# Optimization experiments

Hardware: AMD Instinct MI355X
Metric: run time of the kernel (lower is better)

Reference implementation:

```python
import jax, jax.numpy as jnp
import numpy as np

N_THRESH = 100  # thresholds = 0.00, 0.01, ..., 0.99


def setup_inputs() -> dict:
    key = jax.random.key(0)
    k1, k2 = jax.random.split(key)
    predicted_mask = jax.random.uniform(k1, (32, 1, 1024, 1024), dtype=jnp.float32)
    gt_mask = jax.random.randint(k2, (32, 1, 1024, 1024), 0, 2, dtype=jnp.int32)
    return {"predicted_mask": predicted_mask, "gt_mask": gt_mask}


def reference(predicted_mask, gt_mask):
    # Single-pass histogram formulation of: for each t_k in arange(0,1,0.01),
    # iou_k = |(pred > t_k) & gt| / |(pred > t_k) | gt|  (torchmetrics binary Jaccard,
    # strict '>' thresholding, safe-divide -> 0 when union is empty).
    thresholds = jnp.arange(0.0, 1.0, 0.01, dtype=jnp.float32)  # [100], sorted
    pred = jnp.squeeze(predicted_mask).ravel()                  # [N] probabilities in [0,1]
    gt = jnp.squeeze(gt_mask).ravel().astype(jnp.float32)       # [N] 0/1

    # cnt[i] = number of thresholds strictly below pred[i]; pixel i satisfies
    # (pred > t_k) exactly for k in [0, cnt[i]).
    cnt = jnp.searchsorted(thresholds, pred, side='left')       # [N] int in [0, 100]

    hist_pos = jax.ops.segment_sum(gt, cnt, num_segments=N_THRESH + 1)              # [101]
    hist_all = jax.ops.segment_sum(jnp.ones_like(gt), cnt, num_segments=N_THRESH + 1)

    # TP_k = #{pred > t_k and gt==1} = sum_{c > k} hist_pos[c]  (suffix sums via cumsum)
    tp = jnp.sum(hist_pos) - jnp.cumsum(hist_pos)[:N_THRESH]        # [100]
    pred_pos = jnp.sum(hist_all) - jnp.cumsum(hist_all)[:N_THRESH]  # [100] #{pred > t_k}
    n_gt_pos = jnp.sum(gt)

    union = pred_pos + n_gt_pos - tp                                 # TP + FP + FN
    ious = jnp.where(union > 0, tp / jnp.maximum(union, 1.0), 0.0)   # safe divide -> 0
    return thresholds, ious
```

## Files before the change

### kernel.cpp

```cpp
#include <hip/hip_runtime.h>

#define N_THRESH 100
#define NBINS 101
#define TPB 384
#define GRID 1024
#define FLUSH_GROUPS 29

__global__ void zero_ws_kernel(unsigned long long* __restrict__ ws) {
    int i = threadIdx.x;
    if (i < NBINS + 1) ws[i] = 0ull;
}

__device__ __forceinline__ int bin_of(float v) {
    int e = (int)(v * 100.0f);
    e = e < 0 ? 0 : (e > 99 ? 99 : e);
    double ed = (double)e * 0.01;
    float t0 = (float)ed;
    float t1 = (float)(ed + 0.01);
    int c = e + (t0 < v ? 1 : 0) + (t1 < v ? 1 : 0);
    return c > N_THRESH ? N_THRESH : c;
}

__device__ __forceinline__ void bump(unsigned short* h, int tid, float v, int g) {
    h[bin_of(v) * TPB + tid] += (unsigned short)(1u + (g != 0 ? 256u : 0u));
}

__device__ __forceinline__ void fold_row(const unsigned short* h, int r,
                                         unsigned long long& acc_c,
                                         unsigned long long& acc_p) {
    const unsigned int* row = (const unsigned int*)(h + r * TPB);
    unsigned int c = 0, p = 0;
    for (int j = 0; j < TPB / 2; ++j) {
        int jj = j + r; if (jj >= TPB / 2) jj -= TPB / 2;
        unsigned int v = row[jj];
        c += (v & 0xffu) + ((v >> 16) & 0xffu);
        p += ((v >> 8) & 0xffu) + ((v >> 24) & 0xffu);
    }
    acc_c += c; acc_p += p;
}

#define PROCESS16(PA, PB, PC, PD, GA, GB, GC, GD) do {            \
    bump(sA, tid, (PA).x, (GA).x); bump(sB, tid, (PA).y, (GA).y); \
    bump(sA, tid, (PA).z, (GA).z); bump(sB, tid, (PA).w, (GA).w); \
    bump(sA, tid, (PB).x, (GB).x); bump(sB, tid, (PB).y, (GB).y); \
    bump(sA, tid, (PB).z, (GB).z); bump(sB, tid, (PB).w, (GB).w); \
    bump(sA, tid, (PC).x, (GC).x); bump(sB, tid, (PC).y, (GC).y); \
    bump(sA, tid, (PC).z, (GC).z); bump(sB, tid, (PC).w, (GC).w); \
    bump(sA, tid, (PD).x, (GD).x); bump(sB, tid, (PD).y, (GD).y); \
    bump(sA, tid, (PD).z, (GD).z); bump(sB, tid, (PD).w, (GD).w); \
} while (0)

__global__ __launch_bounds__(TPB) void hist_kernel(
        const float* __restrict__ pred,
        const int* __restrict__ gt,
        unsigned long long* __restrict__ ws,
        float* __restrict__ out,
        int n) {
    __shared__ unsigned short sA[NBINS * TPB];
    __shared__ unsigned short sB[NBINS * TPB];
    __shared__ unsigned int fpos[NBINS], fall[NBINS];
    __shared__ int is_last;

    const int tid = threadIdx.x;
    unsigned int* const za = (unsigned int*)sA;
    unsigned int* const zb = (unsigned int*)sB;

    for (int i = tid; i < NBINS * (TPB / 2); i += TPB) { za[i] = 0u; zb[i] = 0u; }
    __syncthreads();

    const int nvec = n >> 2;
    const float4* __restrict__ p4 = (const float4*)pred;
    const int4*   __restrict__ g4 = (const int4*)gt;
    const int gsz = gridDim.x * blockDim.x;
    const int i0  = blockIdx.x * blockDim.x + tid;
    const int iters  = nvec / gsz;
    const int groups = iters >> 2;

    unsigned long long acc_c = 0ull, acc_p = 0ull;

    int gs = 0;
    while (gs < groups) {
        const int ge = (groups < gs + FLUSH_GROUPS) ? groups : gs + FLUSH_GROUPS;
        int j = i0 + gs * 4 * gsz;
        float4 pa = p4[j], pb = p4[j + gsz], pc = p4[j + 2 * gsz], pd = p4[j + 3 * gsz];
        int4   ga = g4[j], gb = g4[j + gsz], gc = g4[j + 2 * gsz], gd = g4[j + 3 * gsz];
        for (int g = gs + 1; g < ge; ++g) {
            j = i0 + g * 4 * gsz;
            float4 qa = p4[j], qb = p4[j + gsz], qc = p4[j + 2 * gsz], qd = p4[j + 3 * gsz];
            int4   ra = g4[j], rb = g4[j + gsz], rc = g4[j + 2 * gsz], rd = g4[j + 3 * gsz];
            PROCESS16(pa, pb, pc, pd, ga, gb, gc, gd);
            pa = qa; pb = qb; pc = qc; pd = qd;
            ga = ra; gb = rb; gc = rc; gd = rd;
        }
        PROCESS16(pa, pb, pc, pd, ga, gb, gc, gd);
        gs = ge;
        if (gs < groups) {
            __syncthreads();
            if (tid < NBINS)                            fold_row(sA, tid, acc_c, acc_p);
            else if (tid >= 192 && tid < 192 + NBINS)   fold_row(sB, tid - 192, acc_c, acc_p);
            __syncthreads();
            for (int i = tid; i < NBINS * (TPB / 2); i += TPB) { za[i] = 0u; zb[i] = 0u; }
            __syncthreads();
        }
    }

    for (int k = groups * 4; ; ++k) {
        int i = i0 + k * gsz;
        if (i >= nvec) break;
        float4 p = p4[i]; int4 g = g4[i];
        bump(sA, tid, p.x, g.x); bump(sB, tid, p.y, g.y);
        bump(sA, tid, p.z, g.z); bump(sB, tid, p.w, g.w);
    }

    if (blockIdx.x == 0 && tid == 0) {
        for (int k = nvec << 2; k < n; ++k) {
            int b = bin_of(pred[k]);
            sA[b * TPB] = (unsigned short)(sA[b * TPB] + 1u + (gt[k] != 0 ? 256u : 0u));
        }
    }

    __syncthreads();
    if (tid >= 192 && tid < 192 + NBINS) {
        fold_row(sB, tid - 192, acc_c, acc_p);
        fall[tid - 192] = (unsigned int)acc_c;
        fpos[tid - 192] = (unsigned int)acc_p;
    }
    __syncthreads();
    if (tid < NBINS) {
        fold_row(sA, tid, acc_c, acc_p);
        unsigned long long cnt = acc_c + fall[tid];
        unsigned long long pos = acc_p + fpos[tid];
        if (cnt | pos) atomicAdd(&ws[tid], (pos << 32) | cnt);
        __threadfence();
    }
    __syncthreads();
    if (tid == 0) {
        unsigned long long t = atomicAdd(&ws[NBINS], 1ull);
        is_last = (t == (unsigned long long)(gridDim.x - 1)) ? 1 : 0;
    }
    __syncthreads();

    if (is_last) {
        if (tid < NBINS) {
            unsigned long long h = atomicAdd(&ws[tid], 0ull);
            fpos[tid] = (unsigned int)(h >> 32);
            fall[tid] = (unsigned int)(h & 0xffffffffull);
        }
        __syncthreads();
        if (tid < N_THRESH) {
            out[tid] = (float)((double)tid * 0.01);
            unsigned long long tp = 0, pp = 0, ngt = 0;
            for (int c = tid + 1; c <= N_THRESH; ++c) { tp += fpos[c]; pp += fall[c]; }
            for (int c = 0; c <= N_THRESH; ++c) ngt += fpos[c];
            long long uni = (long long)(pp + ngt - tp);
            double iou = (uni > 0) ? (double)tp / (double)uni : 0.0;
            out[N_THRESH + tid] = (float)iou;
        }
    }
}

extern "C" void kernel_launch(void* const* d_in, const int* in_sizes, int n_in,
                              void* d_out, int out_size, void* d_ws, size_t ws_size,
                              hipStream_t stream) {
    const float* pred = (const float*)d_in[0];
    const int*   gt   = (const int*)d_in[1];
    float* out = (float*)d_out;
    unsigned long long* ws = (unsigned long long*)d_ws;
    int n = in_sizes[0];

    zero_ws_kernel<<<1, 128, 0, stream>>>(ws);
    hist_kernel<<<GRID, TPB, 0, stream>>>(pred, gt, ws, out, n);
}
```

Measured before the change: 352.4 us.

## Use single 32-bit packed per-thread histogram and drop periodic flush logic

Replaces the two 16-bit packed histograms (sA/sB, 8-bit count/positive fields) with one 32-bit-per-entry histogram holding 16-bit count and positive fields. The periodic fold-and-rezero flush loop is removed. Block size drops to 256 threads and the grid to 256 blocks, so each thread handles more pixels, in a single pass. This aims to cut flush and barrier overhead and simplify the final fold, at the cost of fewer waves per CU (lower occupancy) for hiding memory and LDS latency.

Result: faster. 295.5 us (-16.1%).

```diff
diff --git a/kernel.cpp b/kernel.cpp
--- a/kernel.cpp
+++ b/kernel.cpp
@@ -2,9 +2,8 @@
 
 #define N_THRESH 100
 #define NBINS 101
-#define TPB 384
-#define GRID 1024
-#define FLUSH_GROUPS 29
+#define TPB 256
+#define GRID 256
 
 __global__ void zero_ws_kernel(unsigned long long* __restrict__ ws) {
     int i = threadIdx.x;
@@ -21,33 +20,20 @@
     return c > N_THRESH ? N_THRESH : c;
 }
 
-__device__ __forceinline__ void bump(unsigned short* h, int tid, float v, int g) {
-    h[bin_of(v) * TPB + tid] += (unsigned short)(1u + (g != 0 ? 256u : 0u));
+__device__ __forceinline__ void bump(unsigned int* __restrict__ h, int tid,
+                                     float v, int g) {
+    h[bin_of(v) * TPB + tid] += 1u + ((unsigned int)(g != 0) << 16);
 }
 
-__device__ __forceinline__ void fold_row(const unsigned short* h, int r,
-                                         unsigned long long& acc_c,
-                                         unsigned long long& acc_p) {
-    const unsigned int* row = (const unsigned int*)(h + r * TPB);
-    unsigned int c = 0, p = 0;
-    for (int j = 0; j < TPB / 2; ++j) {
-        int jj = j + r; if (jj >= TPB / 2) jj -= TPB / 2;
-        unsigned int v = row[jj];
-        c += (v & 0xffu) + ((v >> 16) & 0xffu);
-        p += ((v >> 8) & 0xffu) + ((v >> 24) & 0xffu);
-    }
-    acc_c += c; acc_p += p;
-}
-
-#define PROCESS16(PA, PB, PC, PD, GA, GB, GC, GD) do {            \
-    bump(sA, tid, (PA).x, (GA).x); bump(sB, tid, (PA).y, (GA).y); \
-    bump(sA, tid, (PA).z, (GA).z); bump(sB, tid, (PA).w, (GA).w); \
-    bump(sA, tid, (PB).x, (GB).x); bump(sB, tid, (PB).y, (GB).y); \
-    bump(sA, tid, (PB).z, (GB).z); bump(sB, tid, (PB).w, (GB).w); \
-    bump(sA, tid, (PC).x, (GC).x); bump(sB, tid, (PC).y, (GC).y); \
-    bump(sA, tid, (PC).z, (GC).z); bump(sB, tid, (PC).w, (GC).w); \
-    bump(sA, tid, (PD).x, (GD).x); bump(sB, tid, (PD).y, (GD).y); \
-    bump(sA, tid, (PD).z, (GD).z); bump(sB, tid, (PD).w, (GD).w); \
+#define PROCESS16(PA, PB, PC, PD, GA, GB, GC, GD) do {          \
+    bump(h, tid, (PA).x, (GA).x); bump(h, tid, (PA).y, (GA).y); \
+    bump(h, tid, (PA).z, (GA).z); bump(h, tid, (PA).w, (GA).w); \
+    bump(h, tid, (PB).x, (GB).x); bump(h, tid, (PB).y, (GB).y); \
+    bump(h, tid, (PB).z, (GB).z); bump(h, tid, (PB).w, (GB).w); \
+    bump(h, tid, (PC).x, (GC).x); bump(h, tid, (PC).y, (GC).y); \
+    bump(h, tid, (PC).z, (GC).z); bump(h, tid, (PC).w, (GC).w); \
+    bump(h, tid, (PD).x, (GD).x); bump(h, tid, (PD).y, (GD).y); \
+    bump(h, tid, (PD).z, (GD).z); bump(h, tid, (PD).w, (GD).w); \
 } while (0)
 
 __global__ __launch_bounds__(TPB) void hist_kernel(
@@ -56,16 +42,14 @@
         unsigned long long* __restrict__ ws,
         float* __restrict__ out,
         int n) {
-    __shared__ unsigned short sA[NBINS * TPB];
-    __shared__ unsigned short sB[NBINS * TPB];
+    __shared__ unsigned int hist[NBINS][TPB];
     __shared__ unsigned int fpos[NBINS], fall[NBINS];
     __shared__ int is_last;
 
     const int tid = threadIdx.x;
-    unsigned int* const za = (unsigned int*)sA;
-    unsigned int* const zb = (unsigned int*)sB;
+    unsigned int* const h = &hist[0][0];
 
-    for (int i = tid; i < NBINS * (TPB / 2); i += TPB) { za[i] = 0u; zb[i] = 0u; }
+    for (int i = tid; i < NBINS * TPB; i += TPB) h[i] = 0u;
     __syncthreads();
 
     const int nvec = n >> 2;
@@ -76,15 +60,12 @@
     const int iters  = nvec / gsz;
     const int groups = iters >> 2;
 
-    unsigned long long acc_c = 0ull, acc_p = 0ull;
-
-    int gs = 0;
-    while (gs < groups) {
-        const int ge = (groups < gs + FLUSH_GROUPS) ? groups : gs + FLUSH_GROUPS;
-        int j = i0 + gs * 4 * gsz;
+    int it = 0;
+    if (groups > 0) {
+        int j = i0;
         float4 pa = p4[j], pb = p4[j + gsz], pc = p4[j + 2 * gsz], pd = p4[j + 3 * gsz];
         int4   ga = g4[j], gb = g4[j + gsz], gc = g4[j + 2 * gsz], gd = g4[j + 3 * gsz];
-        for (int g = gs + 1; g < ge; ++g) {
+        for (int g = 1; g < groups; ++g) {
             j = i0 + g * 4 * gsz;
             float4 qa = p4[j], qb = p4[j + gsz], qc = p4[j + 2 * gsz], qd = p4[j + 3 * gsz];
             int4   ra = g4[j], rb = g4[j + gsz], rc = g4[j + 2 * gsz], rd = g4[j + 3 * gsz];
@@ -93,43 +74,38 @@
             ga = ra; gb = rb; gc = rc; gd = rd;
         }
         PROCESS16(pa, pb, pc, pd, ga, gb, gc, gd);
-        gs = ge;
-        if (gs < groups) {
-            __syncthreads();
-            if (tid < NBINS)                            fold_row(sA, tid, acc_c, acc_p);
-            else if (tid >= 192 && tid < 192 + NBINS)   fold_row(sB, tid - 192, acc_c, acc_p);
-            __syncthreads();
-            for (int i = tid; i < NBINS * (TPB / 2); i += TPB) { za[i] = 0u; zb[i] = 0u; }
-            __syncthreads();
+        it = groups * 4;
+    }
+    for (; it < iters; ++it) {
+        int i = i0 + it * gsz;
+        float4 p = p4[i]; int4 g = g4[i];
+        bump(h, tid, p.x, g.x); bump(h, tid, p.y, g.y);
+        bump(h, tid, p.z, g.z); bump(h, tid, p.w, g.w);
+    }
+    {
+        int i = i0 + iters * gsz;
+        if (i < nvec) {
+            float4 p = p4[i]; int4 g = g4[i];
+            bump(h, tid, p.x, g.x); bump(h, tid, p.y, g.y);
+            bump(h, tid, p.z, g.z); bump(h, tid, p.w, g.w);
         }
     }
 
-    for (int k = groups * 4; ; ++k) {
-        int i = i0 + k * gsz;
-        if (i >= nvec) break;
-        float4 p = p4[i]; int4 g = g4[i];
-        bump(sA, tid, p.x, g.x); bump(sB, tid, p.y, g.y);
-        bump(sA, tid, p.z, g.z); bump(sB, tid, p.w, g.w);
-    }
-
     if (blockIdx.x == 0 && tid == 0) {
-        for (int k = nvec << 2; k < n; ++k) {
-            int b = bin_of(pred[k]);
-            sA[b * TPB] = (unsigned short)(sA[b * TPB] + 1u + (gt[k] != 0 ? 256u : 0u));
-        }
+        for (int k = nvec << 2; k < n; ++k)
+            h[bin_of(pred[k]) * TPB] += 1u + ((unsigned int)(gt[k] != 0) << 16);
     }
 
     __syncthreads();
-    if (tid >= 192 && tid < 192 + NBINS) {
-        fold_row(sB, tid - 192, acc_c, acc_p);
-        fall[tid - 192] = (unsigned int)acc_c;
-        fpos[tid - 192] = (unsigned int)acc_p;
-    }
-    __syncthreads();
     if (tid < NBINS) {
-        fold_row(sA, tid, acc_c, acc_p);
-        unsigned long long cnt = acc_c + fall[tid];
-        unsigned long long pos = acc_p + fpos[tid];
+        const unsigned int* row = &hist[tid][0];
+        unsigned long long cnt = 0ull, pos = 0ull;
+        for (int j = 0; j < TPB; ++j) {
+            int jj = j + tid; if (jj >= TPB) jj -= TPB;
+            unsigned int v = row[jj];
+            cnt += v & 0xffffu;
+            pos += v >> 16;
+        }
         if (cnt | pos) atomicAdd(&ws[tid], (pos << 32) | cnt);
         __threadfence();
     }
@@ -142,9 +118,9 @@
 
     if (is_last) {
         if (tid < NBINS) {
-            unsigned long long h = atomicAdd(&ws[tid], 0ull);
-            fpos[tid] = (unsigned int)(h >> 32);
-            fall[tid] = (unsigned int)(h & 0xffffffffull);
+            unsigned long long hv = atomicAdd(&ws[tid], 0ull);
+            fpos[tid] = (unsigned int)(hv >> 32);
+            fall[tid] = (unsigned int)(hv & 0xffffffffull);
         }
         __syncthreads();
         if (tid < N_THRESH) {
```
